# Kernel tuning notes

Measured on AMD Instinct MI355X. Metric: run time of the kernel, lower is better.

The kernel has to match this reference:

```python
import jax, jax.numpy as jnp
import numpy as np

N = 4096        # num_pbits
STEPS = 16384   # sequential single-spin updates (4 sweeps)
BETA = 1.0


def setup_inputs() -> dict:
    key = jax.random.key(0)
    k1, k2, k3, k4 = jax.random.split(key, 4)
    # random_graph: symmetric, zero-diagonal, nonnegative weights; maxcut_J = -W
    U = jax.random.uniform(k1, (N, N), dtype=jnp.float32)
    Wu = jnp.triu(U, 1)
    J = -(Wu + Wu.T)
    h = jnp.zeros((N,), dtype=jnp.float32)
    # initial spins in {-1, +1}
    m0 = jnp.sign(jax.random.normal(k2, (N,), dtype=jnp.float32))
    m0 = jnp.where(m0 == 0, 1.0, m0)
    # pre-drawn per-step RNG: update index and uniform noise in [0,1)
    idx = jax.random.randint(k3, (STEPS,), 0, N, dtype=jnp.int32)
    u = jax.random.uniform(k4, (STEPS,), dtype=jnp.float32)
    return {"J": J, "h": h, "m0": m0, "idx": idx, "u": u}


def reference(J, h, m0, idx, u):
    # Sequential Glauber single p-bit updates (continuous noise).
    def step(m, xs):
        i, ui = xs
        I_i = jnp.dot(J[i], m) + h[i]          # local field, [scalar]
        p_i = jnp.tanh(BETA * I_i)
        r = 2.0 * ui - 1.0                      # uniform in [-1, 1)
        s = jnp.sign(p_i - r)
        s = jnp.where(s == 0, jnp.float32(1.0), s)
        return m.at[i].set(s), None

    m, _ = jax.lax.scan(step, m0, (idx, u))
    return m
```

## Files before the change

kernel.cpp:

```cpp
#include <hip/hip_runtime.h>
#include <math.h>

#define N 4096
#define STEPS 16384
#define WIN 32
#define NWIN (STEPS / WIN)
#define MBLK 1024
#define SBS 36

__device__ __forceinline__ void lgkm_barrier() {
  asm volatile("s_waitcnt lgkmcnt(0)\n\ts_barrier" ::: "memory");
}

__global__ __launch_bounds__(256) void pre_kernel(const float* __restrict__ u,
                                                  const int* __restrict__ idx,
                                                  double* __restrict__ thr,
                                                  int* __restrict__ samemask) {
  int t = blockIdx.x * 256 + threadIdx.x;
  if (t < STEPS) {
    float r = 2.0f * u[t] - 1.0f;
    double rd = (double)r;
    thr[t] = 0.5 * log((1.0 + rd) / (1.0 - rd));
    int cbase = t & ~(WIN - 1);
    int my = idx[t];
    unsigned int sm = 0u;
    for (int q = 0; q < WIN; ++q)
      if (idx[cbase + q] == my) sm |= (1u << q);
    samemask[t] = (int)sm;
  }
}

__global__ __launch_bounds__(256) void init_field_kernel(const float* __restrict__ J,
                                                         const float* __restrict__ h,
                                                         const float* __restrict__ m0,
                                                         double* __restrict__ I) {
  __shared__ double red[256];
  int row = blockIdx.x;
  const float4* Jr = (const float4*)(J + (size_t)row * N);
  const float4* mv = (const float4*)m0;
  double acc = 0.0;
  for (int q = threadIdx.x; q < N / 4; q += 256) {
    float4 a = Jr[q];
    float4 b = mv[q];
    acc += (double)(a.x * b.x) + (double)(a.y * b.y) +
           (double)(a.z * b.z) + (double)(a.w * b.w);
  }
  red[threadIdx.x] = acc;
  __syncthreads();
  for (int s = 128; s > 0; s >>= 1) {
    if (threadIdx.x < s) red[threadIdx.x] += red[threadIdx.x + s];
    __syncthreads();
  }
  if (threadIdx.x == 0) I[row] = red[0] + (double)h[row];
}

__global__ __launch_bounds__(MBLK) void pbit_kernel(const float* __restrict__ J,
                                                    const float* __restrict__ m0,
                                                    const int* __restrict__ idx,
                                                    const double* __restrict__ thr,
                                                    const int* __restrict__ samemask,
                                                    const double* __restrict__ I0,
                                                    float* __restrict__ out) {
  __shared__ __align__(16) double field_lds[N];
  __shared__ __align__(16) float m_lds[N];
  __shared__ __align__(16) float ST_lds[WIN * SBS];
  __shared__ __align__(16) int   pubi_lds[WIN];
  __shared__ __align__(16) float pubd_lds[WIN];
  __shared__ int pubF_lds;

  const int tid = threadIdx.x;

  double i0, i1, i2, i3;
  {
    const double* ip = I0 + 4 * tid;
    i0 = ip[0]; i1 = ip[1]; i2 = ip[2]; i3 = ip[3];
    *(double2*)(field_lds + 4 * tid + 0) = make_double2(i0, i1);
    *(double2*)(field_lds + 4 * tid + 2) = make_double2(i2, i3);
  }
  ((float4*)m_lds)[tid] = ((const float4*)m0)[tid];

  const int t32 = tid & 31;
  const int jrow = tid >> 1;
  const int half = (tid & 1) * 16;

  int mi = 0, ni = 0;
  unsigned int msm = 0u, nsm = 0u;
  double mt = 0.0, nt = 0.0;

  if (tid < 64) {
    mi = idx[t32];       mt = thr[t32];       msm = (unsigned int)samemask[t32];
    ni = idx[WIN + t32]; nt = thr[WIN + t32]; nsm = (unsigned int)samemask[WIN + t32];
    int r0 = __shfl(mi, jrow);
    const float* Jr = J + (size_t)r0 * N;
#pragma unroll
    for (int q = 0; q < 16; ++q) {
      int c = __shfl(mi, half + q);
      ST_lds[jrow * SBS + half + q] = Jr[c];
    }
  }
  __syncthreads();

  for (int k = 0; k < NWIN; ++k) {
    if (tid < 64) {
      int growv = __shfl(ni, jrow);
      const float* Jg = J + (size_t)growv * N;
      int gc0  = __shfl(ni, half + 0),  gc1  = __shfl(ni, half + 1);
      int gc2  = __shfl(ni, half + 2),  gc3  = __shfl(ni, half + 3);
      int gc4  = __shfl(ni, half + 4),  gc5  = __shfl(ni, half + 5);
      int gc6  = __shfl(ni, half + 6),  gc7  = __shfl(ni, half + 7);
      int gc8  = __shfl(ni, half + 8),  gc9  = __shfl(ni, half + 9);
      int gc10 = __shfl(ni, half + 10), gc11 = __shfl(ni, half + 11);
      int gc12 = __shfl(ni, half + 12), gc13 = __shfl(ni, half + 13);
      int gc14 = __shfl(ni, half + 14), gc15 = __shfl(ni, half + 15);
      float gv0  = Jg[gc0],  gv1  = Jg[gc1],  gv2  = Jg[gc2],  gv3  = Jg[gc3];
      float gv4  = Jg[gc4],  gv5  = Jg[gc5],  gv6  = Jg[gc6],  gv7  = Jg[gc7];
      float gv8  = Jg[gc8],  gv9  = Jg[gc9],  gv10 = Jg[gc10], gv11 = Jg[gc11];
      float gv12 = Jg[gc12], gv13 = Jg[gc13], gv14 = Jg[gc14], gv15 = Jg[gc15];
      int b2 = (k + 2) * WIN; if (b2 >= STEPS) b2 = 0;
      int n2i = idx[b2 + t32];
      double n2t = thr[b2 + t32];
      unsigned int n2sm = (unsigned int)samemask[b2 + t32];
      double Ival = field_lds[mi];
      float mcur = m_lds[mi];
      float finals = 0.0f, finald = 0.0f;
      int conf = -1;
      bool locked = false;
      while (true) {
        bool sup = (Ival >= mt);
        float s = sup ? 1.0f : -1.0f;
        float dl = s - mcur;
        unsigned int D = (unsigned int)__ballot(sup);
        unsigned long long mask = __ballot(dl != 0.0f) & 0xFFFFFFFFull;
        mask &= (~0ull) << (conf + 1);
        if (mask == 0) {
          if (!locked) { finals = s; finald = 0.0f; }
          break;
        }
        int f = (int)__builtin_ctzll(mask);
        if (!locked && t32 <= f) { finals = s; finald = dl; locked = true; }
        float s_f  = ((D >> f) & 1u) ? 1.0f : -1.0f;
        float dl_f = 2.0f * s_f;
        float xcol = ST_lds[f * SBS + t32];
        Ival += (double)(xcol * dl_f);
        if ((msm >> f) & 1u) mcur = s_f;
        conf = f;
      }
      unsigned long long fm = __ballot((tid < WIN) && (finald != 0.0f));
      if (tid < WIN) {
        if (finald != 0.0f) {
          int pos = __popcll(fm & ((1ull << t32) - 1ull));
          pubi_lds[pos] = mi;
          pubd_lds[pos] = finald;
        }
        bool mlo = (msm & (0xFFFFFFFEu << t32)) == 0u;
        if (mlo) m_lds[mi] = finals;
        if (tid == 0) pubF_lds = (int)__popcll(fm);
      }
      {
        float* dst = &ST_lds[jrow * SBS + half];
        *(float4*)(dst + 0)  = make_float4(gv0, gv1, gv2, gv3);
        *(float4*)(dst + 4)  = make_float4(gv4, gv5, gv6, gv7);
        *(float4*)(dst + 8)  = make_float4(gv8, gv9, gv10, gv11);
        *(float4*)(dst + 12) = make_float4(gv12, gv13, gv14, gv15);
      }
      mi = ni;  mt = nt;  msm = nsm;
      ni = n2i; nt = n2t; nsm = n2sm;
    }
    lgkm_barrier();

    {
      int F = pubF_lds;
      if (F > 0) {
        const float* Jb = J + 4 * (size_t)tid;
#pragma unroll
        for (int b = 0; b < WIN; b += 8) {
          if (b < F) {
            int4 r1 = *(const int4*)(pubi_lds + b);
            int4 r2 = *(const int4*)(pubi_lds + b + 4);
            float4 d1 = *(const float4*)(pubd_lds + b);
            float4 d2 = *(const float4*)(pubd_lds + b + 4);
            int rr[8] = {r1.x, r1.y, r1.z, r1.w, r2.x, r2.y, r2.z, r2.w};
            float dd[8] = {d1.x, d1.y, d1.z, d1.w, d2.x, d2.y, d2.z, d2.w};
            float4 rv[8];
#pragma unroll
            for (int t = 0; t < 8; ++t)
              if (b + t < F) rv[t] = *(const float4*)(Jb + (size_t)rr[t] * N);
            float a0 = 0.f, a1 = 0.f, a2 = 0.f, a3 = 0.f;
#pragma unroll
            for (int t = 0; t < 8; ++t)
              if (b + t < F) {
                a0 += rv[t].x * dd[t]; a1 += rv[t].y * dd[t];
                a2 += rv[t].z * dd[t]; a3 += rv[t].w * dd[t];
              }
            i0 += (double)a0; i1 += (double)a1;
            i2 += (double)a2; i3 += (double)a3;
          }
        }
        *(double2*)(field_lds + 4 * tid + 0) = make_double2(i0, i1);
        *(double2*)(field_lds + 4 * tid + 2) = make_double2(i2, i3);
      }
    }
    lgkm_barrier();
  }

  __syncthreads();
  ((float4*)out)[tid] = ((const float4*)m_lds)[tid];
}

extern "C" void kernel_launch(void* const* d_in, const int* in_sizes, int n_in,
                              void* d_out, int out_size, void* d_ws, size_t ws_size,
                              hipStream_t stream) {
  const float* J = (const float*)d_in[0];
  const float* h = (const float*)d_in[1];
  const float* m0 = (const float*)d_in[2];
  const int* idx = (const int*)d_in[3];
  const float* u = (const float*)d_in[4];
  float* out = (float*)d_out;

  double* thr = (double*)d_ws;
  double* I0 = (double*)((char*)d_ws + STEPS * sizeof(double));
  int* samemask = (int*)((char*)d_ws + STEPS * sizeof(double)
                                     + N * sizeof(double));

  pre_kernel<<<dim3(STEPS / 256), dim3(256), 0, stream>>>(u, idx, thr, samemask);
  init_field_kernel<<<dim3(N), dim3(256), 0, stream>>>(J, h, m0, I0);
  pbit_kernel<<<dim3(1), dim3(MBLK), 0, stream>>>(J, m0, idx, thr, samemask, I0, out);
}
```

Baseline: 1.622 ms.

## Double-buffer J submatrix tile and prefetch gathers two windows ahead

The 32x32 J submatrix gather for upcoming windows now runs one window further ahead. Registers hold window k+1's values and are written into an alternate LDS buffer at the start of iteration k, while loads for window k+2 are issued. This hides global gather latency behind the serial conflict-resolution loop and the field update, where before the gathered values were needed by the end of the same iteration. The cost is extra registers and LDS, plus a deeper index and threshold prefetch chain.

Measured after the change: 1.623 ms (median of 2 runs). Within noise of the previous version (+0.1%).

```diff
diff --git a/kernel.cpp b/kernel.cpp
--- a/kernel.cpp
+++ b/kernel.cpp
@@ -63,7 +63,7 @@
                                                     float* __restrict__ out) {
   __shared__ __align__(16) double field_lds[N];
   __shared__ __align__(16) float m_lds[N];
-  __shared__ __align__(16) float ST_lds[WIN * SBS];
+  __shared__ __align__(16) float STb[2][WIN * SBS];
   __shared__ __align__(16) int   pubi_lds[WIN];
   __shared__ __align__(16) float pubd_lds[WIN];
   __shared__ int pubF_lds;
@@ -83,43 +83,74 @@
   const int jrow = tid >> 1;
   const int half = (tid & 1) * 16;
 
-  int mi = 0, ni = 0;
-  unsigned int msm = 0u, nsm = 0u;
-  double mt = 0.0, nt = 0.0;
+  int mi = 0, ni = 0, p2i = 0;
+  unsigned int msm = 0u, nsm = 0u, p2sm = 0u;
+  double mt = 0.0, nt = 0.0, p2t = 0.0;
+  float4 gvA, gvB, gvC, gvD;
+  gvA = gvB = gvC = gvD = make_float4(0.f, 0.f, 0.f, 0.f);
 
   if (tid < 64) {
-    mi = idx[t32];       mt = thr[t32];       msm = (unsigned int)samemask[t32];
-    ni = idx[WIN + t32]; nt = thr[WIN + t32]; nsm = (unsigned int)samemask[WIN + t32];
-    int r0 = __shfl(mi, jrow);
-    const float* Jr = J + (size_t)r0 * N;
-#pragma unroll
-    for (int q = 0; q < 16; ++q) {
-      int c = __shfl(mi, half + q);
-      ST_lds[jrow * SBS + half + q] = Jr[c];
+    mi  = idx[t32];           mt  = thr[t32];           msm  = (unsigned int)samemask[t32];
+    ni  = idx[WIN + t32];     nt  = thr[WIN + t32];     nsm  = (unsigned int)samemask[WIN + t32];
+    p2i = idx[2 * WIN + t32]; p2t = thr[2 * WIN + t32]; p2sm = (unsigned int)samemask[2 * WIN + t32];
+    {
+      int r0 = __shfl(mi, jrow);
+      const float* Jr = J + (size_t)r0 * N;
+#pragma unroll
+      for (int q = 0; q < 16; ++q) {
+        int c = __shfl(mi, half + q);
+        STb[0][jrow * SBS + half + q] = Jr[c];
+      }
+    }
+    {
+      int r1 = __shfl(ni, jrow);
+      const float* Jg = J + (size_t)r1 * N;
+      int c0  = __shfl(ni, half + 0),  c1  = __shfl(ni, half + 1);
+      int c2  = __shfl(ni, half + 2),  c3  = __shfl(ni, half + 3);
+      int c4  = __shfl(ni, half + 4),  c5  = __shfl(ni, half + 5);
+      int c6  = __shfl(ni, half + 6),  c7  = __shfl(ni, half + 7);
+      int c8  = __shfl(ni, half + 8),  c9  = __shfl(ni, half + 9);
+      int c10 = __shfl(ni, half + 10), c11 = __shfl(ni, half + 11);
+      int c12 = __shfl(ni, half + 12), c13 = __shfl(ni, half + 13);
+      int c14 = __shfl(ni, half + 14), c15 = __shfl(ni, half + 15);
+      gvA = make_float4(Jg[c0],  Jg[c1],  Jg[c2],  Jg[c3]);
+      gvB = make_float4(Jg[c4],  Jg[c5],  Jg[c6],  Jg[c7]);
+      gvC = make_float4(Jg[c8],  Jg[c9],  Jg[c10], Jg[c11]);
+      gvD = make_float4(Jg[c12], Jg[c13], Jg[c14], Jg[c15]);
     }
   }
   __syncthreads();
 
   for (int k = 0; k < NWIN; ++k) {
     if (tid < 64) {
-      int growv = __shfl(ni, jrow);
-      const float* Jg = J + (size_t)growv * N;
-      int gc0  = __shfl(ni, half + 0),  gc1  = __shfl(ni, half + 1);
-      int gc2  = __shfl(ni, half + 2),  gc3  = __shfl(ni, half + 3);
-      int gc4  = __shfl(ni, half + 4),  gc5  = __shfl(ni, half + 5);
-      int gc6  = __shfl(ni, half + 6),  gc7  = __shfl(ni, half + 7);
-      int gc8  = __shfl(ni, half + 8),  gc9  = __shfl(ni, half + 9);
-      int gc10 = __shfl(ni, half + 10), gc11 = __shfl(ni, half + 11);
-      int gc12 = __shfl(ni, half + 12), gc13 = __shfl(ni, half + 13);
-      int gc14 = __shfl(ni, half + 14), gc15 = __shfl(ni, half + 15);
-      float gv0  = Jg[gc0],  gv1  = Jg[gc1],  gv2  = Jg[gc2],  gv3  = Jg[gc3];
-      float gv4  = Jg[gc4],  gv5  = Jg[gc5],  gv6  = Jg[gc6],  gv7  = Jg[gc7];
-      float gv8  = Jg[gc8],  gv9  = Jg[gc9],  gv10 = Jg[gc10], gv11 = Jg[gc11];
-      float gv12 = Jg[gc12], gv13 = Jg[gc13], gv14 = Jg[gc14], gv15 = Jg[gc15];
-      int b2 = (k + 2) * WIN; if (b2 >= STEPS) b2 = 0;
-      int n2i = idx[b2 + t32];
-      double n2t = thr[b2 + t32];
-      unsigned int n2sm = (unsigned int)samemask[b2 + t32];
+      {
+        float* dst = &STb[(k + 1) & 1][jrow * SBS + half];
+        *(float4*)(dst + 0)  = gvA;
+        *(float4*)(dst + 4)  = gvB;
+        *(float4*)(dst + 8)  = gvC;
+        *(float4*)(dst + 12) = gvD;
+      }
+      {
+        int grow = __shfl(p2i, jrow);
+        const float* Jg = J + (size_t)grow * N;
+        int c0  = __shfl(p2i, half + 0),  c1  = __shfl(p2i, half + 1);
+        int c2  = __shfl(p2i, half + 2),  c3  = __shfl(p2i, half + 3);
+        int c4  = __shfl(p2i, half + 4),  c5  = __shfl(p2i, half + 5);
+        int c6  = __shfl(p2i, half + 6),  c7  = __shfl(p2i, half + 7);
+        int c8  = __shfl(p2i, half + 8),  c9  = __shfl(p2i, half + 9);
+        int c10 = __shfl(p2i, half + 10), c11 = __shfl(p2i, half + 11);
+        int c12 = __shfl(p2i, half + 12), c13 = __shfl(p2i, half + 13);
+        int c14 = __shfl(p2i, half + 14), c15 = __shfl(p2i, half + 15);
+        gvA = make_float4(Jg[c0],  Jg[c1],  Jg[c2],  Jg[c3]);
+        gvB = make_float4(Jg[c4],  Jg[c5],  Jg[c6],  Jg[c7]);
+        gvC = make_float4(Jg[c8],  Jg[c9],  Jg[c10], Jg[c11]);
+        gvD = make_float4(Jg[c12], Jg[c13], Jg[c14], Jg[c15]);
+      }
+      int b3 = (k + 3) * WIN; if (b3 >= STEPS) b3 = 0;
+      int n3i = idx[b3 + t32];
+      double n3t = thr[b3 + t32];
+      unsigned int n3sm = (unsigned int)samemask[b3 + t32];
+      const float* SB = &STb[k & 1][0];
       double Ival = field_lds[mi];
       float mcur = m_lds[mi];
       float finals = 0.0f, finald = 0.0f;
@@ -140,7 +171,7 @@
         if (!locked && t32 <= f) { finals = s; finald = dl; locked = true; }
         float s_f  = ((D >> f) & 1u) ? 1.0f : -1.0f;
         float dl_f = 2.0f * s_f;
-        float xcol = ST_lds[f * SBS + t32];
+        float xcol = SB[f * SBS + t32];
         Ival += (double)(xcol * dl_f);
         if ((msm >> f) & 1u) mcur = s_f;
         conf = f;
@@ -156,15 +187,9 @@
         if (mlo) m_lds[mi] = finals;
         if (tid == 0) pubF_lds = (int)__popcll(fm);
       }
-      {
-        float* dst = &ST_lds[jrow * SBS + half];
-        *(float4*)(dst + 0)  = make_float4(gv0, gv1, gv2, gv3);
-        *(float4*)(dst + 4)  = make_float4(gv4, gv5, gv6, gv7);
-        *(float4*)(dst + 8)  = make_float4(gv8, gv9, gv10, gv11);
-        *(float4*)(dst + 12) = make_float4(gv12, gv13, gv14, gv15);
-      }
-      mi = ni;  mt = nt;  msm = nsm;
-      ni = n2i; nt = n2t; nsm = n2sm;
+      mi  = ni;  mt  = nt;  msm  = nsm;
+      ni  = p2i; nt  = p2t; nsm  = p2sm;
+      p2i = n3i; p2t = n3t; p2sm = n3sm;
     }
     lgkm_barrier();
 
```

## Widen speculative update window to 64 steps with double-buffered J sub-tile

Applied to the files above, without the earlier changes.

Doubles the speculative window from 32 to 64 steps, so one full wave64 resolves the window and the same-index masks become 64-bit. This halves the number of block-wide barrier rounds and field-update passes. The 64x64 J sub-tile is double-buffered in LDS and its gather is split into two halves, one overlapped with conflict resolution and one with the field update. In exchange, the serial conflict-resolution loop can run more iterations per window, more rows are summed per update, and LDS and workspace use grow.

After: 2.812 ms. +73.3%, slower.

```diff
diff --git a/kernel.cpp b/kernel.cpp
--- a/kernel.cpp
+++ b/kernel.cpp
@@ -3,10 +3,10 @@
 
 #define N 4096
 #define STEPS 16384
-#define WIN 32
+#define WIN 64
 #define NWIN (STEPS / WIN)
 #define MBLK 1024
-#define SBS 36
+#define SBS64 65
 
 __device__ __forceinline__ void lgkm_barrier() {
   asm volatile("s_waitcnt lgkmcnt(0)\n\ts_barrier" ::: "memory");
@@ -15,7 +15,7 @@
 __global__ __launch_bounds__(256) void pre_kernel(const float* __restrict__ u,
                                                   const int* __restrict__ idx,
                                                   double* __restrict__ thr,
-                                                  int* __restrict__ samemask) {
+                                                  unsigned long long* __restrict__ samemask) {
   int t = blockIdx.x * 256 + threadIdx.x;
   if (t < STEPS) {
     float r = 2.0f * u[t] - 1.0f;
@@ -23,10 +23,10 @@
     thr[t] = 0.5 * log((1.0 + rd) / (1.0 - rd));
     int cbase = t & ~(WIN - 1);
     int my = idx[t];
-    unsigned int sm = 0u;
+    unsigned long long sm = 0ull;
     for (int q = 0; q < WIN; ++q)
-      if (idx[cbase + q] == my) sm |= (1u << q);
-    samemask[t] = (int)sm;
+      if (idx[cbase + q] == my) sm |= (1ull << q);
+    samemask[t] = sm;
   }
 }
 
@@ -58,12 +58,12 @@
                                                     const float* __restrict__ m0,
                                                     const int* __restrict__ idx,
                                                     const double* __restrict__ thr,
-                                                    const int* __restrict__ samemask,
+                                                    const unsigned long long* __restrict__ samemask,
                                                     const double* __restrict__ I0,
                                                     float* __restrict__ out) {
   __shared__ __align__(16) double field_lds[N];
   __shared__ __align__(16) float m_lds[N];
-  __shared__ __align__(16) float ST_lds[WIN * SBS];
+  __shared__ __align__(16) float STb[2][WIN * SBS64];
   __shared__ __align__(16) int   pubi_lds[WIN];
   __shared__ __align__(16) float pubd_lds[WIN];
   __shared__ int pubF_lds;
@@ -79,47 +79,55 @@
   }
   ((float4*)m_lds)[tid] = ((const float4*)m0)[tid];
 
-  const int t32 = tid & 31;
-  const int jrow = tid >> 1;
-  const int half = (tid & 1) * 16;
+  const int t64 = tid & 63;
+  const int grow_r = tid >> 1;
+  const int ghalf = (tid & 1) * 32;
 
   int mi = 0, ni = 0;
-  unsigned int msm = 0u, nsm = 0u;
+  unsigned long long msm = 0ull, nsm = 0ull;
   double mt = 0.0, nt = 0.0;
+  float gva[32];
+#pragma unroll
+  for (int q = 0; q < 32; ++q) gva[q] = 0.f;
 
   if (tid < 64) {
-    mi = idx[t32];       mt = thr[t32];       msm = (unsigned int)samemask[t32];
-    ni = idx[WIN + t32]; nt = thr[WIN + t32]; nsm = (unsigned int)samemask[WIN + t32];
-    int r0 = __shfl(mi, jrow);
-    const float* Jr = J + (size_t)r0 * N;
-#pragma unroll
-    for (int q = 0; q < 16; ++q) {
-      int c = __shfl(mi, half + q);
-      ST_lds[jrow * SBS + half + q] = Jr[c];
+    mi = idx[t64];       mt = thr[t64];       msm = samemask[t64];
+    ni = idx[WIN + t64]; nt = thr[WIN + t64]; nsm = samemask[WIN + t64];
+    {
+      int rowA = __shfl(mi, grow_r);
+      const float* Ja = J + (size_t)rowA * N;
+#pragma unroll
+      for (int q = 0; q < 32; ++q) {
+        int c = __shfl(mi, ghalf + q);
+        STb[0][grow_r * SBS64 + ghalf + q] = Ja[c];
+      }
+      int rowB = __shfl(mi, 32 + grow_r);
+      const float* Jc = J + (size_t)rowB * N;
+#pragma unroll
+      for (int q = 0; q < 32; ++q) {
+        int c = __shfl(mi, ghalf + q);
+        STb[0][(32 + grow_r) * SBS64 + ghalf + q] = Jc[c];
+      }
     }
   }
   __syncthreads();
 
   for (int k = 0; k < NWIN; ++k) {
     if (tid < 64) {
-      int growv = __shfl(ni, jrow);
-      const float* Jg = J + (size_t)growv * N;
-      int gc0  = __shfl(ni, half + 0),  gc1  = __shfl(ni, half + 1);
-      int gc2  = __shfl(ni, half + 2),  gc3  = __shfl(ni, half + 3);
-      int gc4  = __shfl(ni, half + 4),  gc5  = __shfl(ni, half + 5);
-      int gc6  = __shfl(ni, half + 6),  gc7  = __shfl(ni, half + 7);
-      int gc8  = __shfl(ni, half + 8),  gc9  = __shfl(ni, half + 9);
-      int gc10 = __shfl(ni, half + 10), gc11 = __shfl(ni, half + 11);
-      int gc12 = __shfl(ni, half + 12), gc13 = __shfl(ni, half + 13);
-      int gc14 = __shfl(ni, half + 14), gc15 = __shfl(ni, half + 15);
-      float gv0  = Jg[gc0],  gv1  = Jg[gc1],  gv2  = Jg[gc2],  gv3  = Jg[gc3];
-      float gv4  = Jg[gc4],  gv5  = Jg[gc5],  gv6  = Jg[gc6],  gv7  = Jg[gc7];
-      float gv8  = Jg[gc8],  gv9  = Jg[gc9],  gv10 = Jg[gc10], gv11 = Jg[gc11];
-      float gv12 = Jg[gc12], gv13 = Jg[gc13], gv14 = Jg[gc14], gv15 = Jg[gc15];
+      {
+        int rowA = __shfl(ni, grow_r);
+        const float* Jg = J + (size_t)rowA * N;
+#pragma unroll
+        for (int q = 0; q < 32; ++q) {
+          int c = __shfl(ni, ghalf + q);
+          gva[q] = Jg[c];
+        }
+      }
       int b2 = (k + 2) * WIN; if (b2 >= STEPS) b2 = 0;
-      int n2i = idx[b2 + t32];
-      double n2t = thr[b2 + t32];
-      unsigned int n2sm = (unsigned int)samemask[b2 + t32];
+      int n2i = idx[b2 + t64];
+      double n2t = thr[b2 + t64];
+      unsigned long long n2sm = samemask[b2 + t64];
+      const float* SB = &STb[k & 1][0];
       double Ival = field_lds[mi];
       float mcur = m_lds[mi];
       float finals = 0.0f, finald = 0.0f;
@@ -129,39 +137,47 @@
         bool sup = (Ival >= mt);
         float s = sup ? 1.0f : -1.0f;
         float dl = s - mcur;
-        unsigned int D = (unsigned int)__ballot(sup);
-        unsigned long long mask = __ballot(dl != 0.0f) & 0xFFFFFFFFull;
-        mask &= (~0ull) << (conf + 1);
-        if (mask == 0) {
+        unsigned long long D = __ballot(sup);
+        unsigned long long mask = __ballot(dl != 0.0f);
+        unsigned long long gate = (conf >= 63) ? 0ull : ((~0ull) << (conf + 1));
+        mask &= gate;
+        if (mask == 0ull) {
           if (!locked) { finals = s; finald = 0.0f; }
           break;
         }
         int f = (int)__builtin_ctzll(mask);
-        if (!locked && t32 <= f) { finals = s; finald = dl; locked = true; }
-        float s_f  = ((D >> f) & 1u) ? 1.0f : -1.0f;
+        if (!locked && t64 <= f) { finals = s; finald = dl; locked = true; }
+        float s_f  = ((D >> f) & 1ull) ? 1.0f : -1.0f;
         float dl_f = 2.0f * s_f;
-        float xcol = ST_lds[f * SBS + t32];
+        float xcol = SB[f * SBS64 + t64];
         Ival += (double)(xcol * dl_f);
-        if ((msm >> f) & 1u) mcur = s_f;
+        if ((msm >> f) & 1ull) mcur = s_f;
         conf = f;
       }
-      unsigned long long fm = __ballot((tid < WIN) && (finald != 0.0f));
-      if (tid < WIN) {
+      unsigned long long fm = __ballot(finald != 0.0f);
+      {
         if (finald != 0.0f) {
-          int pos = __popcll(fm & ((1ull << t32) - 1ull));
+          int pos = (int)__popcll(fm & ((1ull << t64) - 1ull));
           pubi_lds[pos] = mi;
           pubd_lds[pos] = finald;
         }
-        bool mlo = (msm & (0xFFFFFFFEu << t32)) == 0u;
+        bool mlo = ((msm >> t64) >> 1) == 0ull;
         if (mlo) m_lds[mi] = finals;
         if (tid == 0) pubF_lds = (int)__popcll(fm);
       }
       {
-        float* dst = &ST_lds[jrow * SBS + half];
-        *(float4*)(dst + 0)  = make_float4(gv0, gv1, gv2, gv3);
-        *(float4*)(dst + 4)  = make_float4(gv4, gv5, gv6, gv7);
-        *(float4*)(dst + 8)  = make_float4(gv8, gv9, gv10, gv11);
-        *(float4*)(dst + 12) = make_float4(gv12, gv13, gv14, gv15);
+        float* dst = &STb[(k + 1) & 1][grow_r * SBS64 + ghalf];
+#pragma unroll
+        for (int q = 0; q < 32; ++q) dst[q] = gva[q];
+      }
+      {
+        int rowB = __shfl(ni, 32 + grow_r);
+        const float* Jg = J + (size_t)rowB * N;
+#pragma unroll
+        for (int q = 0; q < 32; ++q) {
+          int c = __shfl(ni, ghalf + q);
+          gva[q] = Jg[c];
+        }
       }
       mi = ni;  mt = nt;  msm = nsm;
       ni = n2i; nt = n2t; nsm = n2sm;
@@ -199,6 +215,11 @@
         *(double2*)(field_lds + 4 * tid + 0) = make_double2(i0, i1);
         *(double2*)(field_lds + 4 * tid + 2) = make_double2(i2, i3);
       }
+      if (tid < 64) {
+        float* dst = &STb[(k + 1) & 1][(32 + grow_r) * SBS64 + ghalf];
+#pragma unroll
+        for (int q = 0; q < 32; ++q) dst[q] = gva[q];
+      }
     }
     lgkm_barrier();
   }
@@ -219,8 +240,9 @@
 
   double* thr = (double*)d_ws;
   double* I0 = (double*)((char*)d_ws + STEPS * sizeof(double));
-  int* samemask = (int*)((char*)d_ws + STEPS * sizeof(double)
-                                     + N * sizeof(double));
+  unsigned long long* samemask =
+      (unsigned long long*)((char*)d_ws + STEPS * sizeof(double)
+                                        + N * sizeof(double));
 
   pre_kernel<<<dim3(STEPS / 256), dim3(256), 0, stream>>>(u, idx, thr, samemask);
   init_field_kernel<<<dim3(N), dim3(256), 0, stream>>>(J, h, m0, I0);
```
